# Performance work log

Measured on AMD Instinct MI355X. Metric: run time of the kernel, lower is better.

## Reference

```python
import jax, jax.numpy as jnp
import numpy as np

N_NODES = 50000
IN_DIM = 256
OUT_DIM = 128
NUM_HEADS = 2
N_EDGES = 800000


def setup_inputs() -> dict:
    key = jax.random.key(0)
    k1, k2, k3, k4, k5 = jax.random.split(key, 5)
    x = jax.random.normal(k1, (N_NODES, IN_DIM), dtype=jnp.float32)
    edge_index = jax.random.randint(k2, (2, N_EDGES), 0, N_NODES, dtype=jnp.int64)
    # Linear(in_dim, out_dim*num_heads): store weight as [in_dim, out_dim*num_heads]
    fan = IN_DIM + OUT_DIM * NUM_HEADS
    W_w = jax.random.uniform(k3, (IN_DIM, OUT_DIM * NUM_HEADS), dtype=jnp.float32,
                             minval=-np.sqrt(6.0 / fan), maxval=np.sqrt(6.0 / fan))
    W_b = jnp.zeros((OUT_DIM * NUM_HEADS,), dtype=jnp.float32)
    # attention vector a: [2*out_dim], xavier uniform over (1, 2*out_dim)
    fa = 1 + 2 * OUT_DIM
    a = jax.random.uniform(k4, (2 * OUT_DIM,), dtype=jnp.float32,
                           minval=-np.sqrt(6.0 / fa), maxval=np.sqrt(6.0 / fa))
    return {"x": x, "edge_index": edge_index, "W_w": W_w, "W_b": W_b, "a": a}


def _gat_forward(x, edge_index, W_w, W_b, a):
    N = x.shape[0]
    H, D = NUM_HEADS, OUT_DIM
    Wh = (x @ W_w + W_b).reshape(N, H, D)  # [N, H, D]
    src, dst = edge_index[0], edge_index[1]
    a_src, a_dst = a[:D], a[D:]
    # per-node partial scores, then gather -> avoids [E, 2D] concat
    s = jnp.einsum('nhd,d->nh', Wh, a_src)  # [N, H]
    t = jnp.einsum('nhd,d->nh', Wh, a_dst)  # [N, H]
    e = jax.nn.leaky_relu(s[src] + t[dst], negative_slope=0.2)  # [E, H]
    # segment softmax over edges grouped by src node
    m = jax.ops.segment_max(e, src, num_segments=N)  # [N, H], -inf for empty
    ex = jnp.exp(e - m[src])
    denom = jax.ops.segment_sum(ex, src, num_segments=N)  # [N, H]
    alpha = ex / denom[src]  # [E, H]
    # weighted aggregation of destination features into source nodes
    agg = jax.ops.segment_sum(alpha[:, :, None] * Wh[dst], src, num_segments=N)  # [N, H, D]
    deg = jax.ops.segment_sum(jnp.ones_like(src, dtype=Wh.dtype), src, num_segments=N)  # [N]
    h_prime = jnp.where(deg[:, None, None] > 0, agg, Wh)
    return h_prime.reshape(N, H * D)


def reference(x, edge_index, W_w, W_b, a):
    return _gat_forward(x, edge_index, W_w, W_b, a)
```

## Files before the change

### kernel.cpp

```cpp
#include <hip/hip_runtime.h>
#include <hip/hip_bf16.h>
#include <math.h>

#define N_NODES 50000
#define IN_DIM 256
#define OUT_DIM 128
#define NUM_HEADS 2
#define N_EDGES 800000
#define F (OUT_DIM*NUM_HEADS)
#define SCAN_B 1024
#define N_SB ((N_NODES + SCAN_B - 1) / SCAN_B)
#define LDSP 264
#define CAP 128
#define N_COPIES 8

typedef __bf16 bf16;
typedef __bf16 bf16x8 __attribute__((ext_vector_type(8)));
typedef float  f32x4  __attribute__((ext_vector_type(4)));

__global__ void k_transpose(const float* __restrict__ W, bf16* __restrict__ Wt,
                            int* __restrict__ deg8) {
    int k = blockIdx.x;
    int n = threadIdx.x;
    Wt[(size_t)n*IN_DIM + k] = (bf16)W[(size_t)k*F + n];
    int id = blockIdx.x * F + threadIdx.x;
    for (int i = id; i < N_COPIES * N_NODES; i += IN_DIM * F)
        deg8[i] = 0;
}

__global__ __launch_bounds__(256) void k_gemm(const float* __restrict__ X,
                                              const bf16* __restrict__ Wt,
                                              const float* __restrict__ Wb,
                                              const float* __restrict__ Av,
                                              const int* __restrict__ src,
                                              int* __restrict__ deg8,
                                              bf16* __restrict__ Wh,
                                              float* __restrict__ s_arr,
                                              float* __restrict__ t_arr) {
    __shared__ bf16 As[64 * LDSP];
    __shared__ float sS[2][64], sT[2][64];
    int t = threadIdx.x;
    int wave = t >> 6, lane = t & 63;
    int quad = lane >> 4, l16 = lane & 15;
    int row0 = blockIdx.x * 64;
    int col0 = wave * 64;
    int h = wave >> 1;

    {
        int gid = blockIdx.x * 256 + t;
        int gsz = gridDim.x * 256;
        int* mydeg = deg8 + (size_t)(blockIdx.x & (N_COPIES - 1)) * N_NODES;
        for (int e = gid; e < N_EDGES; e += gsz)
            atomicAdd(&mydeg[src[e]], 1);
    }

    {
        int rr = t >> 5;
        int cc = (t & 31) * 8;
        #pragma unroll
        for (int i = 0; i < 8; ++i) {
            int r = row0 + 8*i + rr;
            r = (r < N_NODES) ? r : (N_NODES - 1);
            const float* p = X + (size_t)r * IN_DIM + cc;
            f32x4 lo = *(const f32x4*)p;
            f32x4 hi = *(const f32x4*)(p + 4);
            bf16x8 pk;
            #pragma unroll
            for (int q = 0; q < 4; ++q) {
                pk[q]   = (bf16)lo[q];
                pk[q+4] = (bf16)hi[q];
            }
            *(bf16x8*)(As + (8*i + rr) * LDSP + cc) = pk;
        }
    }
    if (t < 128) { sS[t >> 6][t & 63] = 0.f; sT[t >> 6][t & 63] = 0.f; }
    __syncthreads();

    f32x4 acc[4][4] = {};
    #pragma unroll
    for (int ks = 0; ks < 8; ++ks) {
        int kb = ks * 32;
        bf16x8 bfrag[4];
        #pragma unroll
        for (int ni = 0; ni < 4; ++ni)
            bfrag[ni] = *(const bf16x8*)(Wt + (size_t)(col0 + ni*16 + l16)*IN_DIM
                                            + kb + quad*8);
        bf16x8 afrag[4];
        #pragma unroll
        for (int mi = 0; mi < 4; ++mi)
            afrag[mi] = *(const bf16x8*)(As + (mi*16 + l16)*LDSP + kb + quad*8);

        #pragma unroll
        for (int mi = 0; mi < 4; ++mi)
            #pragma unroll
            for (int ni = 0; ni < 4; ++ni)
                acc[mi][ni] = __builtin_amdgcn_mfma_f32_16x16x32_bf16(
                                  afrag[mi], bfrag[ni], acc[mi][ni], 0, 0, 0);
    }

    float bias_l[4], as_l[4], at_l[4];
    #pragma unroll
    for (int ni = 0; ni < 4; ++ni) {
        int c = col0 + ni*16 + l16;
        int d = c & (OUT_DIM - 1);
        bias_l[ni] = Wb[c];
        as_l[ni]   = Av[d];
        at_l[ni]   = Av[OUT_DIM + d];
    }

    #pragma unroll
    for (int mi = 0; mi < 4; ++mi) {
        #pragma unroll
        for (int reg = 0; reg < 4; ++reg) {
            int rl = mi*16 + quad*4 + reg;
            float ps = 0.f, pt = 0.f;
            #pragma unroll
            for (int ni = 0; ni < 4; ++ni) {
                float val = acc[mi][ni][reg] + bias_l[ni];
                ps += val * as_l[ni];
                pt += val * at_l[ni];
            }
            #pragma unroll
            for (int m = 8; m >= 1; m >>= 1) {
                ps += __shfl_xor(ps, m);
                pt += __shfl_xor(pt, m);
            }
            if ((lane & 15) == 0) {
                atomicAdd(&sS[h][rl], ps);
                atomicAdd(&sT[h][rl], pt);
            }
        }
    }

    __syncthreads();
    #pragma unroll
    for (int mi = 0; mi < 4; ++mi)
        #pragma unroll
        for (int ni = 0; ni < 4; ++ni) {
            int cc = col0 + ni*16 + l16;
            #pragma unroll
            for (int reg = 0; reg < 4; ++reg) {
                int rl = mi*16 + quad*4 + reg;
                As[rl*LDSP + cc] = (bf16)(acc[mi][ni][reg] + bias_l[ni]);
            }
        }
    __syncthreads();

    #pragma unroll
    for (int i = 0; i < 8; ++i) {
        int idx = i * 2048 + t * 8;
        int row = idx >> 8;
        int cc  = idx & 255;
        bf16x8 v = *(const bf16x8*)(As + row*LDSP + cc);
        int grow = row0 + row;
        if (grow < N_NODES)
            *(bf16x8*)(Wh + (size_t)grow*F + cc) = v;
    }

    if (t < 128) {
        int hh = t >> 6, rl = t & 63;
        int n = row0 + rl;
        if (n < N_NODES) {
            s_arr[n*2 + hh] = sS[hh][rl];
            t_arr[n*2 + hh] = sT[hh][rl];
        }
    }
}

__global__ __launch_bounds__(SCAN_B) void k_scan_local(const int* __restrict__ deg8,
                                                       int* __restrict__ excl,
                                                       int* __restrict__ bsum) {
    __shared__ int lds[SCAN_B];
    int t = threadIdx.x;
    int i = blockIdx.x * SCAN_B + t;
    int v = 0;
    if (i < N_NODES) {
        #pragma unroll
        for (int c = 0; c < N_COPIES; ++c)
            v += deg8[(size_t)c * N_NODES + i];
    }
    lds[t] = v;
    __syncthreads();
    for (int off = 1; off < SCAN_B; off <<= 1) {
        int u = (t >= off) ? lds[t - off] : 0;
        __syncthreads();
        lds[t] += u;
        __syncthreads();
    }
    if (i < N_NODES) excl[i] = lds[t] - v;
    if (t == SCAN_B - 1) bsum[blockIdx.x] = lds[t];
}

__global__ __launch_bounds__(256) void k_scan_final(const int* __restrict__ excl,
                                                    const int* __restrict__ bsum,
                                                    int* __restrict__ row_start,
                                                    int* __restrict__ cursor) {
    __shared__ int sboff[64];
    int t = threadIdx.x;
    if (t < 64) {
        int orig = (t < N_SB) ? bsum[t] : 0;
        int v = orig;
        #pragma unroll
        for (int off = 1; off < 64; off <<= 1) {
            int u = __shfl_up(v, off);
            if (t >= off) v += u;
        }
        sboff[t] = v - orig;
        if (t == 63 && blockIdx.x == 0) row_start[N_NODES] = v;
    }
    __syncthreads();
    int i = blockIdx.x * 256 + t;
    if (i < N_NODES) {
        int e0 = excl[i] + sboff[i >> 10];
        row_start[i] = e0;
        cursor[i]    = e0;
    }
}

__global__ void k_scatter(const int* __restrict__ src, const int* __restrict__ dst,
                          int* __restrict__ cursor, int* __restrict__ sorted_dst) {
    int e = blockIdx.x * 256 + threadIdx.x;
    if (e < N_EDGES) {
        int s = src[e];
        int pos = atomicAdd(&cursor[s], 1);
        sorted_dst[pos] = dst[e];
    }
}

__global__ __launch_bounds__(256) void k_agg(const bf16* __restrict__ Wh,
                                             const float* __restrict__ s_arr,
                                             const float* __restrict__ t_arr,
                                             const int* __restrict__ row_start,
                                             const int* __restrict__ sdst,
                                             float* __restrict__ out) {
    __shared__ float sp0[4][CAP];
    __shared__ float sp1[4][CAP];
    __shared__ int   sd[4][CAP];
    int wave = threadIdx.x >> 6, lane = threadIdx.x & 63;
    int n = blockIdx.x * 4 + wave;
    int sub = lane >> 5, cl = lane & 31;
    int c = cl * 8, h = cl >> 4;
    int beg = row_start[n], end = row_start[n + 1];
    if (beg == end) {
        if (sub == 0) {
            bf16x8 wh = *(const bf16x8*)(Wh + (size_t)n*F + c);
            f32x4 o0, o1;
            #pragma unroll
            for (int i = 0; i < 4; ++i) { o0[i] = (float)wh[i]; o1[i] = (float)wh[4+i]; }
            *(f32x4*)(out + (size_t)n*F + c)     = o0;
            *(f32x4*)(out + (size_t)n*F + c + 4) = o1;
        }
        return;
    }
    float2 sv = ((const float2*)s_arr)[n];
    float sum0 = 0.f, sum1 = 0.f;
    float a[8] = {0,0,0,0,0,0,0,0};
    float bacc[8] = {0,0,0,0,0,0,0,0};
    const float* sph = h ? sp1[wave] : sp0[wave];

    for (int c0 = beg; c0 < end; c0 += CAP) {
        int cnt = min(CAP, end - c0);
        for (int j = lane; j < cnt; j += 64) {
            int d = sdst[c0 + j];
            float2 tv = ((const float2*)t_arr)[d];
            float e0 = sv.x + tv.x; e0 = (e0 >= 0.f) ? e0 : 0.2f * e0;
            float e1 = sv.y + tv.y; e1 = (e1 >= 0.f) ? e1 : 0.2f * e1;
            float p0 = __expf(e0), p1 = __expf(e1);
            sp0[wave][j] = p0;
            sp1[wave][j] = p1;
            sd[wave][j]  = d;
            sum0 += p0;
            sum1 += p1;
        }
        int j = 0;
        for (; j + 8 <= cnt; j += 8) {
            int j0 = j + sub, j1 = j + 2 + sub, j2 = j + 4 + sub, j3 = j + 6 + sub;
            int d0 = sd[wave][j0], d1 = sd[wave][j1];
            int d2 = sd[wave][j2], d3 = sd[wave][j3];
            float p0 = sph[j0], p1 = sph[j1], p2 = sph[j2], p3 = sph[j3];
            bf16x8 w0 = *(const bf16x8*)(Wh + (size_t)d0*F + c);
            bf16x8 w1 = *(const bf16x8*)(Wh + (size_t)d1*F + c);
            bf16x8 w2 = *(const bf16x8*)(Wh + (size_t)d2*F + c);
            bf16x8 w3 = *(const bf16x8*)(Wh + (size_t)d3*F + c);
            #pragma unroll
            for (int i = 0; i < 8; ++i) {
                a[i]    += p0 * (float)w0[i];
                bacc[i] += p1 * (float)w1[i];
                a[i]    += p2 * (float)w2[i];
                bacc[i] += p3 * (float)w3[i];
            }
        }
        for (; j < cnt; j += 2) {
            int jj = j + sub;
            int jc = (jj < cnt) ? jj : 0;
            float p = (jj < cnt) ? sph[jc] : 0.f;
            int d = sd[wave][jc];
            bf16x8 w = *(const bf16x8*)(Wh + (size_t)d*F + c);
            #pragma unroll
            for (int i = 0; i < 8; ++i) a[i] += p * (float)w[i];
        }
    }
    #pragma unroll
    for (int m = 32; m >= 1; m >>= 1) {
        sum0 += __shfl_xor(sum0, m);
        sum1 += __shfl_xor(sum1, m);
    }
    float inv = 1.f / (h ? sum1 : sum0);
    #pragma unroll
    for (int i = 0; i < 8; ++i) {
        a[i] += bacc[i];
        a[i] += __shfl_xor(a[i], 32);
    }
    if (sub == 0) {
        f32x4 o0, o1;
        #pragma unroll
        for (int i = 0; i < 4; ++i) { o0[i] = a[i] * inv; o1[i] = a[4+i] * inv; }
        *(f32x4*)(out + (size_t)n*F + c)     = o0;
        *(f32x4*)(out + (size_t)n*F + c + 4) = o1;
    }
}

extern "C" void kernel_launch(void* const* d_in, const int* in_sizes, int n_in,
                              void* d_out, int out_size, void* d_ws, size_t ws_size,
                              hipStream_t stream) {
    const float* x  = (const float*)d_in[0];
    const int*   ei = (const int*)d_in[1];
    const float* Ww = (const float*)d_in[2];
    const float* Wb = (const float*)d_in[3];
    const float* a  = (const float*)d_in[4];
    float* out = (float*)d_out;
    const int* src = ei;
    const int* dst = ei + N_EDGES;

    char* ws = (char*)d_ws;
    bf16*  Wh        = (bf16*)ws;   ws += (size_t)N_NODES * F * 2;
    bf16*  Wt        = (bf16*)ws;   ws += (size_t)IN_DIM * F * 2;
    float* s_arr     = (float*)ws;  ws += (size_t)N_NODES * 2 * 4;
    float* t_arr     = (float*)ws;  ws += (size_t)N_NODES * 2 * 4;
    int*   excl      = (int*)ws;    ws += (size_t)N_NODES * 4;
    int*   bsum      = (int*)ws;    ws += 64 * 4;
    int*   row_start = (int*)ws;    ws += (size_t)(N_NODES + 1) * 4 + 12;
    int*   cursor    = (int*)ws;    ws += (size_t)N_NODES * 4;
    int*   sdst      = (int*)ws;    ws += (size_t)N_EDGES * 4;

    int* deg8 = sdst;

    k_transpose<<<IN_DIM, F, 0, stream>>>(Ww, Wt, deg8);
    k_gemm<<<(N_NODES + 63) / 64, 256, 0, stream>>>(x, Wt, Wb, a, src, deg8,
                                                    Wh, s_arr, t_arr);
    k_scan_local<<<N_SB, SCAN_B, 0, stream>>>(deg8, excl, bsum);
    k_scan_final<<<(N_NODES + 255) / 256, 256, 0, stream>>>(excl, bsum, row_start, cursor);
    k_scatter<<<(N_EDGES + 255) / 256, 256, 0, stream>>>(src, dst, cursor, sdst);
    k_agg<<<N_NODES / 4, 256, 0, stream>>>(Wh, s_arr, t_arr, row_start, sdst, out);
}
```

Measured before the change: 263.7 us.

## Use per-XCD degree copies with ranks to replace scatter atomics

```diff
diff --git a/kernel.cpp b/kernel.cpp
--- a/kernel.cpp
+++ b/kernel.cpp
@@ -13,10 +13,13 @@
 #define LDSP 264
 #define CAP 128
 #define N_COPIES 8
+#define NBLK ((N_NODES + 63) / 64)
+#define GSZ (NBLK * 256)
 
 typedef __bf16 bf16;
 typedef __bf16 bf16x8 __attribute__((ext_vector_type(8)));
 typedef float  f32x4  __attribute__((ext_vector_type(4)));
+typedef unsigned short u16x8 __attribute__((ext_vector_type(8)));
 
 __global__ void k_transpose(const float* __restrict__ W, bf16* __restrict__ Wt,
                             int* __restrict__ deg8) {
@@ -34,6 +37,8 @@
                                               const float* __restrict__ Av,
                                               const int* __restrict__ src,
                                               int* __restrict__ deg8,
+                                              unsigned char* __restrict__ rank,
+                                              int* __restrict__ xcdtab,
                                               bf16* __restrict__ Wh,
                                               float* __restrict__ s_arr,
                                               float* __restrict__ t_arr) {
@@ -47,11 +52,18 @@
     int h = wave >> 1;
 
     {
+        unsigned xcc;
+        asm volatile("s_getreg_b32 %0, hwreg(HW_REG_XCC_ID, 0, 4)" : "=s"(xcc));
+        xcc &= (N_COPIES - 1);
+        if (t == 0) xcdtab[blockIdx.x] = (int)xcc;
+        int* mydeg = deg8 + (size_t)xcc * N_NODES;
         int gid = blockIdx.x * 256 + t;
-        int gsz = gridDim.x * 256;
-        int* mydeg = deg8 + (size_t)(blockIdx.x & (N_COPIES - 1)) * N_NODES;
-        for (int e = gid; e < N_EDGES; e += gsz)
-            atomicAdd(&mydeg[src[e]], 1);
+        for (int e = gid; e < N_EDGES; e += GSZ) {
+            int s = src[e];
+            int r = __hip_atomic_fetch_add(&mydeg[s], 1, __ATOMIC_RELAXED,
+                                           __HIP_MEMORY_SCOPE_WORKGROUP);
+            rank[e] = (unsigned char)r;
+        }
     }
 
     {
@@ -169,15 +181,22 @@
 
 __global__ __launch_bounds__(SCAN_B) void k_scan_local(const int* __restrict__ deg8,
                                                        int* __restrict__ excl,
-                                                       int* __restrict__ bsum) {
+                                                       int* __restrict__ bsum,
+                                                       unsigned short* __restrict__ prefix8) {
     __shared__ int lds[SCAN_B];
     int t = threadIdx.x;
     int i = blockIdx.x * SCAN_B + t;
     int v = 0;
     if (i < N_NODES) {
-        #pragma unroll
-        for (int c = 0; c < N_COPIES; ++c)
-            v += deg8[(size_t)c * N_NODES + i];
+        u16x8 pf;
+        int run = 0;
+        #pragma unroll
+        for (int c = 0; c < N_COPIES; ++c) {
+            pf[c] = (unsigned short)run;
+            run += deg8[(size_t)c * N_NODES + i];
+        }
+        v = run;
+        *(u16x8*)(prefix8 + (size_t)i * 8) = pf;
     }
     lds[t] = v;
     __syncthreads();
@@ -193,8 +212,7 @@
 
 __global__ __launch_bounds__(256) void k_scan_final(const int* __restrict__ excl,
                                                     const int* __restrict__ bsum,
-                                                    int* __restrict__ row_start,
-                                                    int* __restrict__ cursor) {
+                                                    int* __restrict__ row_start) {
     __shared__ int sboff[64];
     int t = threadIdx.x;
     if (t < 64) {
@@ -210,19 +228,22 @@
     }
     __syncthreads();
     int i = blockIdx.x * 256 + t;
-    if (i < N_NODES) {
-        int e0 = excl[i] + sboff[i >> 10];
-        row_start[i] = e0;
-        cursor[i]    = e0;
-    }
-}
-
-__global__ void k_scatter(const int* __restrict__ src, const int* __restrict__ dst,
-                          int* __restrict__ cursor, int* __restrict__ sorted_dst) {
+    if (i < N_NODES)
+        row_start[i] = excl[i] + sboff[i >> 10];
+}
+
+__global__ __launch_bounds__(256) void k_scatter(const int* __restrict__ src,
+                                                 const int* __restrict__ dst,
+                                                 const unsigned char* __restrict__ rank,
+                                                 const unsigned short* __restrict__ prefix8,
+                                                 const int* __restrict__ row_start,
+                                                 const int* __restrict__ xcdtab,
+                                                 int* __restrict__ sorted_dst) {
     int e = blockIdx.x * 256 + threadIdx.x;
     if (e < N_EDGES) {
+        int c = xcdtab[(e % GSZ) >> 8];
         int s = src[e];
-        int pos = atomicAdd(&cursor[s], 1);
+        int pos = row_start[s] + (int)prefix8[(size_t)s * 8 + c] + (int)rank[e];
         sorted_dst[pos] = dst[e];
     }
 }
@@ -340,16 +361,19 @@
     int*   excl      = (int*)ws;    ws += (size_t)N_NODES * 4;
     int*   bsum      = (int*)ws;    ws += 64 * 4;
     int*   row_start = (int*)ws;    ws += (size_t)(N_NODES + 1) * 4 + 12;
-    int*   cursor    = (int*)ws;    ws += (size_t)N_NODES * 4;
+    unsigned short* prefix8 = (unsigned short*)ws; ws += (size_t)N_NODES * 8 * 2;
+    unsigned char*  rank    = (unsigned char*)ws;  ws += (size_t)N_EDGES + 16;
+    int*   xcdtab    = (int*)ws;    ws += (size_t)NBLK * 4 + 8;
     int*   sdst      = (int*)ws;    ws += (size_t)N_EDGES * 4;
 
     int* deg8 = sdst;
 
     k_transpose<<<IN_DIM, F, 0, stream>>>(Ww, Wt, deg8);
-    k_gemm<<<(N_NODES + 63) / 64, 256, 0, stream>>>(x, Wt, Wb, a, src, deg8,
-                                                    Wh, s_arr, t_arr);
-    k_scan_local<<<N_SB, SCAN_B, 0, stream>>>(deg8, excl, bsum);
-    k_scan_final<<<(N_NODES + 255) / 256, 256, 0, stream>>>(excl, bsum, row_start, cursor);
-    k_scatter<<<(N_EDGES + 255) / 256, 256, 0, stream>>>(src, dst, cursor, sdst);
+    k_gemm<<<NBLK, 256, 0, stream>>>(x, Wt, Wb, a, src, deg8, rank, xcdtab,
+                                     Wh, s_arr, t_arr);
+    k_scan_local<<<N_SB, SCAN_B, 0, stream>>>(deg8, excl, bsum, prefix8);
+    k_scan_final<<<(N_NODES + 255) / 256, 256, 0, stream>>>(excl, bsum, row_start);
+    k_scatter<<<(N_EDGES + 255) / 256, 256, 0, stream>>>(src, dst, rank, prefix8,
+                                                         row_start, xcdtab, sdst);
     k_agg<<<N_NODES / 4, 256, 0, stream>>>(Wh, s_arr, t_arr, row_start, sdst, out);
 }
```

Measured after the change: 244.9 us. -7.1%, faster.
